# Optimization experiments

Hardware: AMD Instinct MI355X
Metric: run time of the kernel (lower is better)

The kernel has to match this reference:

```python
import jax, jax.numpy as jnp
import numpy as np

B, L, D = 2, 2048, 2048
HQ, HKV = 32, 8
HD = D // HQ            # 64
G = HQ // HKV           # 4


def setup_inputs() -> dict:
    key = jax.random.key(0)
    ks = jax.random.split(key, 9)
    s = 1.0 / np.sqrt(D)
    return {
        "x": jax.random.normal(ks[0], (B, L, D), jnp.float32),
        "Wq": jax.random.normal(ks[1], (D, HQ * HD), jnp.float32) * s,
        "bq": jnp.zeros((HQ * HD,), jnp.float32),
        "Wk": jax.random.normal(ks[2], (D, HKV * HD), jnp.float32) * s,
        "bk": jnp.zeros((HKV * HD,), jnp.float32),
        "Wv": jax.random.normal(ks[3], (D, HKV * HD), jnp.float32) * s,
        "bv": jnp.zeros((HKV * HD,), jnp.float32),
        "Wo": jax.random.normal(ks[4], (HQ * HD, D), jnp.float32) * s,
        "bo": jnp.zeros((D,), jnp.float32),
    }


def reference(x, Wq, bq, Wk, bk, Wv, bv, Wo, bo):
    # projections
    q = x @ Wq + bq                                   # [B, L, HQ*HD]
    k = x @ Wk + bk                                   # [B, L, HKV*HD]
    v = x @ Wv + bv
    # split heads; group q heads by kv head: [B, HKV, G, L, HD]
    q = q.reshape(B, L, HKV, G, HD).transpose(0, 2, 3, 1, 4)
    k = k.reshape(B, L, HKV, HD).transpose(0, 2, 1, 3)   # [B, HKV, L, HD]
    v = v.reshape(B, L, HKV, HD).transpose(0, 2, 1, 3)
    scale = 1.0 / np.sqrt(HD)
    # scores [B, HKV, G, Lq, Lk] -- same math as repeat_kv + matmul
    scores = jnp.einsum('bhgqd,bhkd->bhgqk', q, k) * scale
    attn = jax.nn.softmax(scores, axis=-1)
    ctx = jnp.einsum('bhgqk,bhkd->bhgqd', attn, v)       # [B, HKV, G, L, HD]
    # merge heads back to [B, L, HQ*HD]
    ctx = ctx.transpose(0, 3, 1, 2, 4).reshape(B, L, HQ * HD)
    return ctx @ Wo + bo
```

## Files before the change

### kernel.cpp

```cpp
#include <hip/hip_runtime.h>
#include <cstdint>
#include <cstring>


#define L_SEQ 2048
#define D_MODEL 2048
#define M_ROWS 4096
#define KV_COLS 512
#define ATTN_SCALE 0.18033688011112042f

typedef __bf16 bf16x8 __attribute__((ext_vector_type(8)));
typedef float f32x4 __attribute__((ext_vector_type(4)));
typedef float f32x16 __attribute__((ext_vector_type(16)));

__device__ __forceinline__ f32x4 zero4() {
    f32x4 v; v[0] = 0.f; v[1] = 0.f; v[2] = 0.f; v[3] = 0.f; return v;
}

__device__ __forceinline__ unsigned short f2bf(float x) {
    unsigned u = __builtin_bit_cast(unsigned, x);
    u = (u + 0x7FFFu + ((u >> 16) & 1u)) >> 16;
    return (unsigned short)u;
}

__device__ __forceinline__ unsigned pk_bf16(float a, float b) {
#if __has_builtin(__builtin_amdgcn_cvt_pk_bf16_f32)
    typedef __bf16 bf16x2 __attribute__((ext_vector_type(2)));
    bf16x2 r = __builtin_amdgcn_cvt_pk_bf16_f32(a, b);
    return __builtin_bit_cast(unsigned, r);
#else
    return (unsigned)f2bf(a) | ((unsigned)f2bf(b) << 16);
#endif
}

__device__ __forceinline__ f32x4 mfma16(uint4 a, uint4 b, f32x4 c) {
    return __builtin_amdgcn_mfma_f32_16x16x32_bf16(
        __builtin_bit_cast(bf16x8, a), __builtin_bit_cast(bf16x8, b), c, 0, 0, 0);
}
__device__ __forceinline__ f32x16 mfma32(uint4 a, uint4 b, f32x16 c) {
    return __builtin_amdgcn_mfma_f32_32x32x16_bf16(
        __builtin_bit_cast(bf16x8, a), __builtin_bit_cast(bf16x8, b), c, 0, 0, 0);
}

__device__ __forceinline__ void gl_lds16(const unsigned short* g, unsigned short* l) {
    __builtin_amdgcn_global_load_lds(
        (const __attribute__((address_space(1))) unsigned int*)g,
        (__attribute__((address_space(3))) unsigned int*)l, 16, 0, 0);
}

#if __has_builtin(__builtin_amdgcn_exp2f)
#define EXP2F(x) __builtin_amdgcn_exp2f(x)
#else
#define EXP2F(x) exp2f(x)
#endif


__global__ __launch_bounds__(256) void cast_x_kernel(const float* __restrict__ in,
                                                     unsigned short* __restrict__ out,
                                                     int n4) {
    int i = blockIdx.x * 256 + threadIdx.x;
    if (i >= n4) return;
    float4 v = ((const float4*)in)[i];
    uint2 o;
    o.x = pk_bf16(v.x, v.y);
    o.y = pk_bf16(v.z, v.w);
    ((uint2*)out)[i] = o;
}

__global__ __launch_bounds__(256) void transpose_cast_kernel(const float* __restrict__ in,
                                                             unsigned short* __restrict__ out,
                                                             int N, int row_off) {
    __shared__ float tile[32][33];
    const int n0 = blockIdx.x * 32, k0 = blockIdx.y * 32;
    const int tc = threadIdx.x & 31, tr = threadIdx.x >> 5;
#pragma unroll
    for (int i = 0; i < 4; ++i)
        tile[tr + i * 8][tc] = in[(size_t)(k0 + tr + i * 8) * N + n0 + tc];
    __syncthreads();
#pragma unroll
    for (int i = 0; i < 4; ++i)
        out[(size_t)(row_off + n0 + tr + i * 8) * 2048 + k0 + tc] = f2bf(tile[tc][tr + i * 8]);
}

__global__ __launch_bounds__(256) void transpose_v_kernel(const unsigned short* __restrict__ Vb,
                                                          unsigned short* __restrict__ Vt) {
    __shared__ unsigned short tile[32][33];
    const int c0 = blockIdx.x * 32, l0 = blockIdx.y * 32, b = blockIdx.z;
    const int tc = threadIdx.x & 31, tr = threadIdx.x >> 5;
#pragma unroll
    for (int i = 0; i < 4; ++i)
        tile[tr + i * 8][tc] = Vb[(size_t)(b * 2048 + l0 + tr + i * 8) * KV_COLS + c0 + tc];
    __syncthreads();
#pragma unroll
    for (int i = 0; i < 4; ++i)
        Vt[(size_t)(b * 512 + c0 + tr + i * 8) * 2048 + l0 + tc] = tile[tc][tr + i * 8];
}


__device__ __forceinline__ void gemm_core_2048(const unsigned short* __restrict__ A,
                                               const unsigned short* __restrict__ Bt,
                                               int m_block, int n_block,
                                               unsigned short* smA, unsigned short* smB,
                                               f32x4 acc[4][4]) {
    const int tid = threadIdx.x;
    const int w = tid >> 6, lane = tid & 63;
    const int wm = w >> 1, wn = w & 1;
    const int lr = lane & 15, lg = lane >> 4;

#pragma unroll
    for (int i = 0; i < 4; ++i)
#pragma unroll
        for (int j = 0; j < 4; ++j) acc[i][j] = zero4();

    const int rowA = m_block * 128 + w * 32 + (lane >> 2);
    const int rowB = n_block * 128 + w * 32 + (lane >> 2);
    const int kcol = (lane & 3) * 8;
    const unsigned short* gA0 = A + (size_t)rowA * 2048 + kcol;
    const unsigned short* gA1 = gA0 + (size_t)16 * 2048;
    const unsigned short* gB0 = Bt + (size_t)rowB * 2048 + kcol;
    const unsigned short* gB1 = gB0 + (size_t)16 * 2048;
    unsigned short* lA0 = smA + (w * 32) * 32;
    unsigned short* lA1 = smA + (w * 32 + 16) * 32;
    unsigned short* lB0 = smB + (w * 32) * 32;
    unsigned short* lB1 = smB + (w * 32 + 16) * 32;

    for (int kt = 0; kt < 64; ++kt) {
        gl_lds16(gA0 + kt * 32, lA0);
        gl_lds16(gA1 + kt * 32, lA1);
        gl_lds16(gB0 + kt * 32, lB0);
        gl_lds16(gB1 + kt * 32, lB1);
        __syncthreads();
        uint4 af[4], bfg[4];
#pragma unroll
        for (int i = 0; i < 4; ++i)
            af[i] = *(const uint4*)(smA + (wm * 64 + i * 16 + lr) * 32 + lg * 8);
#pragma unroll
        for (int j = 0; j < 4; ++j)
            bfg[j] = *(const uint4*)(smB + (wn * 64 + j * 16 + lr) * 32 + lg * 8);
#pragma unroll
        for (int i = 0; i < 4; ++i)
#pragma unroll
            for (int j = 0; j < 4; ++j)
                acc[i][j] = mfma16(af[i], bfg[j], acc[i][j]);
        __syncthreads();
    }
}

__global__ __launch_bounds__(256) void gemm_qkv_kernel(
    const unsigned short* __restrict__ Xb, const unsigned short* __restrict__ Wt,
    const float* __restrict__ bq, const float* __restrict__ bk, const float* __restrict__ bv,
    unsigned short* __restrict__ Qb, unsigned short* __restrict__ Kb,
    unsigned short* __restrict__ Vb) {
    __shared__ __align__(16) unsigned short smA[128 * 32];
    __shared__ __align__(16) unsigned short smB[128 * 32];
    f32x4 acc[4][4];
    gemm_core_2048(Xb, Wt, blockIdx.x, blockIdx.y, smA, smB, acc);

    const int tid = threadIdx.x;
    const int w = tid >> 6, lane = tid & 63;
    const int wm = w >> 1, wn = w & 1;
    const int lr = lane & 15, lg = lane >> 4;
    const int nbase = blockIdx.y * 128;

    unsigned short* outp; int ldo, noff; const float* bias; float scale;
    if (nbase < 2048)      { outp = Qb; ldo = 2048; noff = 0;    bias = bq; scale = 1.f; }
    else if (nbase < 2560) { outp = Kb; ldo = 512;  noff = 2048; bias = bk; scale = ATTN_SCALE; }
    else                   { outp = Vb; ldo = 512;  noff = 2560; bias = bv; scale = 1.f; }

#pragma unroll
    for (int i = 0; i < 4; ++i) {
        const int mrow = blockIdx.x * 128 + wm * 64 + i * 16 + lg * 4;
#pragma unroll
        for (int j = 0; j < 4; ++j) {
            const int nloc = nbase + wn * 64 + j * 16 + lr - noff;
            const float bb = bias[nloc];
#pragma unroll
            for (int r = 0; r < 4; ++r)
                outp[(size_t)(mrow + r) * ldo + nloc] = f2bf((acc[i][j][r] + bb) * scale);
        }
    }
}

__global__ __launch_bounds__(256) void gemm_out_kernel(
    const unsigned short* __restrict__ Cb, const unsigned short* __restrict__ Wot,
    const float* __restrict__ bo, float* __restrict__ out) {
    __shared__ __align__(16) unsigned short smA[128 * 32];
    __shared__ __align__(16) unsigned short smB[128 * 32];
    f32x4 acc[4][4];
    gemm_core_2048(Cb, Wot, blockIdx.x, blockIdx.y, smA, smB, acc);

    const int tid = threadIdx.x;
    const int w = tid >> 6, lane = tid & 63;
    const int wm = w >> 1, wn = w & 1;
    const int lr = lane & 15, lg = lane >> 4;

#pragma unroll
    for (int i = 0; i < 4; ++i) {
        const int mrow = blockIdx.x * 128 + wm * 64 + i * 16 + lg * 4;
#pragma unroll
        for (int j = 0; j < 4; ++j) {
            const int ncol = blockIdx.y * 128 + wn * 64 + j * 16 + lr;
            const float bb = bo[ncol];
#pragma unroll
            for (int r = 0; r < 4; ++r)
                out[(size_t)(mrow + r) * 2048 + ncol] = acc[i][j][r] + bb;
        }
    }
}


__global__ __launch_bounds__(256, 2) void attn_kernel(const unsigned short* __restrict__ Qb,
                                                      const unsigned short* __restrict__ Kb,
                                                      const unsigned short* __restrict__ Vtg,
                                                      unsigned short* __restrict__ ctx) {
    __shared__ __align__(16) unsigned short smem[16384];
    unsigned short* ks = smem;
    unsigned short* vt = smem + 8192;

    const int qt = blockIdx.x, hq = blockIdx.y, b = blockIdx.z;
    const int kvh = hq >> 2;
    const int tid = threadIdx.x;
    const int w = tid >> 6, lane = tid & 63;
    const int l31 = lane & 31, h = lane >> 5;

    const int qbase = qt * 256 + w * 64;
    uint4 qf[2][4];
#pragma unroll
    for (int u = 0; u < 2; ++u) {
        const unsigned short* qp =
            Qb + (size_t)(b * L_SEQ + qbase + u * 32 + l31) * 2048 + hq * 64;
#pragma unroll
        for (int dh = 0; dh < 4; ++dh)
            qf[u][dh] = *(const uint4*)(qp + dh * 16 + h * 8);
    }

    f32x16 o00, o01, o10, o11;
#pragma unroll
    for (int r = 0; r < 16; ++r) { o00[r] = 0.f; o01[r] = 0.f; o10[r] = 0.f; o11[r] = 0.f; }
    float l_acc0 = 0.f, l_acc1 = 0.f;

    const size_t kbase = (size_t)(b * L_SEQ) * KV_COLS + kvh * 64;
    const size_t vbase = (size_t)((b * 8 + kvh) * 64) * 2048;

    const int rrk = lane >> 3, cpk = lane & 7;
    const int drv = lane >> 4, cpv = lane & 15;

    for (int t = 0; t < 16; ++t) {
        const int k0 = t * 128;
#pragma unroll
        for (int s = 0; s < 4; ++s) {
            const int blkk = w * 4 + s;
            gl_lds16(Kb + kbase + (size_t)(k0 + blkk * 8 + rrk) * KV_COLS + ((cpk ^ rrk) * 8),
                     ks + blkk * 512);
            const int blkv = w * 4 + s;
            const int d = blkv * 4 + drv;
            gl_lds16(Vtg + vbase + (size_t)d * 2048 + k0 + ((cpv ^ (d & 15)) * 8),
                     vt + blkv * 512);
        }
        __syncthreads();

#pragma unroll
        for (int c = 0; c < 4; ++c) {
            uint4 kf[4];
#pragma unroll
            for (int dh = 0; dh < 4; ++dh)
                kf[dh] = *(const uint4*)&ks[(c * 32 + l31) * 64 +
                                            (((dh * 2 + h) ^ (l31 & 7)) * 8)];
            unsigned E0[4][2], E1[4][2];
#pragma unroll
            for (int u = 0; u < 2; ++u) {
                f32x16 s;
#pragma unroll
                for (int r = 0; r < 16; ++r) s[r] = 0.f;
#pragma unroll
                for (int dh = 0; dh < 4; ++dh) s = mfma32(kf[dh], qf[u][dh], s);
                float lsum = 0.f;
#pragma unroll
                for (int g = 0; g < 4; ++g) {
                    float e0 = EXP2F(s[4 * g + 0]);
                    float e1 = EXP2F(s[4 * g + 1]);
                    float e2 = EXP2F(s[4 * g + 2]);
                    float e3 = EXP2F(s[4 * g + 3]);
                    lsum += (e0 + e1) + (e2 + e3);
                    if (u == 0) { E0[g][0] = pk_bf16(e0, e1); E0[g][1] = pk_bf16(e2, e3); }
                    else        { E1[g][0] = pk_bf16(e0, e1); E1[g][1] = pk_bf16(e2, e3); }
                }
                if (u == 0) l_acc0 += lsum; else l_acc1 += lsum;
            }
            const int posv = (c * 4) ^ (l31 & 15);
#pragma unroll
            for (int tau = 0; tau < 2; ++tau) {
                const int pos = ((c * 4 + tau * 2 + h) ^ (l31 & 15)) * 8;
                uint4 vf0 = *(const uint4*)&vt[(size_t)l31 * 128 + pos];
                uint4 vf1 = *(const uint4*)&vt[(size_t)(32 + l31) * 128 + pos];
                {
                    unsigned pub0 = h ? E0[2 * tau][0] : E0[2 * tau + 1][0];
                    unsigned pub1 = h ? E0[2 * tau][1] : E0[2 * tau + 1][1];
                    unsigned R0 = (unsigned)__shfl_xor((int)pub0, 32, 64);
                    unsigned R1 = (unsigned)__shfl_xor((int)pub1, 32, 64);
                    uint4 pf;
                    pf.x = h ? R0 : E0[2 * tau][0];
                    pf.y = h ? R1 : E0[2 * tau][1];
                    pf.z = h ? E0[2 * tau + 1][0] : R0;
                    pf.w = h ? E0[2 * tau + 1][1] : R1;
                    o00 = mfma32(vf0, pf, o00);
                    o01 = mfma32(vf1, pf, o01);
                }
                {
                    unsigned pub0 = h ? E1[2 * tau][0] : E1[2 * tau + 1][0];
                    unsigned pub1 = h ? E1[2 * tau][1] : E1[2 * tau + 1][1];
                    unsigned R0 = (unsigned)__shfl_xor((int)pub0, 32, 64);
                    unsigned R1 = (unsigned)__shfl_xor((int)pub1, 32, 64);
                    uint4 pf;
                    pf.x = h ? R0 : E1[2 * tau][0];
                    pf.y = h ? R1 : E1[2 * tau][1];
                    pf.z = h ? E1[2 * tau + 1][0] : R0;
                    pf.w = h ? E1[2 * tau + 1][1] : R1;
                    o10 = mfma32(vf0, pf, o10);
                    o11 = mfma32(vf1, pf, o11);
                }
            }
            (void)posv;
        }
        __syncthreads();
    }

    __syncthreads();
    unsigned* ep = (unsigned*)smem + w * 1088;
#pragma unroll
    for (int u = 0; u < 2; ++u) {
        const float la = u ? l_acc1 : l_acc0;
        const float l_tot = la + __shfl_xor(la, 32, 64);
        const float rl = 1.f / l_tot;
#pragma unroll
        for (int dt = 0; dt < 2; ++dt) {
            const f32x16& o = u ? (dt ? o11 : o10) : (dt ? o01 : o00);
#pragma unroll
            for (int g = 0; g < 4; ++g)
#pragma unroll
                for (int p = 0; p < 2; ++p) {
                    const int dv = dt * 16 + 4 * g + 2 * h + p;
                    ep[l31 * 34 + dv] =
                        pk_bf16(o[4 * g + 2 * p] * rl, o[4 * g + 2 * p + 1] * rl);
                }
        }
        __builtin_amdgcn_s_waitcnt(0);
#pragma unroll
        for (int p = 0; p < 4; ++p) {
            const int qr = (lane >> 3) + p * 8;
            const int cch = lane & 7;
            uint4 vv = *(const uint4*)((const unsigned short*)ep + qr * 68 + cch * 8);
            *(uint4*)(ctx + (size_t)(b * L_SEQ + qbase + u * 32 + qr) * 2048 +
                      hq * 64 + cch * 8) = vv;
        }
        __builtin_amdgcn_s_waitcnt(0);
    }
}


extern "C" void kernel_launch(void* const* d_in, const int* in_sizes, int n_in,
                              void* d_out, int out_size, void* d_ws, size_t ws_size,
                              hipStream_t stream) {
    const float* x  = (const float*)d_in[0];
    const float* Wq = (const float*)d_in[1];
    const float* bq = (const float*)d_in[2];
    const float* Wk = (const float*)d_in[3];
    const float* bk = (const float*)d_in[4];
    const float* Wv = (const float*)d_in[5];
    const float* bv = (const float*)d_in[6];
    const float* Wo = (const float*)d_in[7];
    const float* bo = (const float*)d_in[8];
    float* out = (float*)d_out;

    char* ws = (char*)d_ws;
    size_t off = 0;
    auto alloc = [&](size_t bytes) {
        char* p = ws + off;
        off += (bytes + 255) & ~(size_t)255;
        return p;
    };
    unsigned short* Wqkvt = (unsigned short*)alloc((size_t)3072 * 2048 * 2);
    unsigned short* Wot   = (unsigned short*)alloc((size_t)2048 * 2048 * 2);
    unsigned short* Xb    = (unsigned short*)alloc((size_t)M_ROWS * 2048 * 2);
    unsigned short* Qb    = (unsigned short*)alloc((size_t)M_ROWS * 2048 * 2);
    unsigned short* Kb    = (unsigned short*)alloc((size_t)M_ROWS * KV_COLS * 2);
    unsigned short* Vb    = (unsigned short*)alloc((size_t)M_ROWS * KV_COLS * 2);
    unsigned short* Vt    = (unsigned short*)alloc((size_t)M_ROWS * KV_COLS * 2);
    unsigned short* Cb    = Xb;

    cast_x_kernel<<<(M_ROWS * 2048 / 4 + 255) / 256, 256, 0, stream>>>(x, Xb,
                                                                       M_ROWS * 2048 / 4);
    transpose_cast_kernel<<<dim3(64, 64), 256, 0, stream>>>(Wq, Wqkvt, 2048, 0);
    transpose_cast_kernel<<<dim3(16, 64), 256, 0, stream>>>(Wk, Wqkvt, 512, 2048);
    transpose_cast_kernel<<<dim3(16, 64), 256, 0, stream>>>(Wv, Wqkvt, 512, 2560);
    transpose_cast_kernel<<<dim3(64, 64), 256, 0, stream>>>(Wo, Wot, 2048, 0);
    gemm_qkv_kernel<<<dim3(32, 24), 256, 0, stream>>>(Xb, Wqkvt, bq, bk, bv, Qb, Kb, Vb);
    transpose_v_kernel<<<dim3(16, 64, 2), 256, 0, stream>>>(Vb, Vt);
    attn_kernel<<<dim3(8, 32, 2), 256, 0, stream>>>(Qb, Kb, Vt, Cb);
    gemm_out_kernel<<<dim3(32, 16), 256, 0, stream>>>(Cb, Wot, bo, out);
}
```

Before: 348.3 us.

## Double-buffer K/V tiles in attention and split query rows across 8 waves

The attention kernel now runs 512 threads per block, each wave handling 32 query rows instead of 64. This halves the per-wave accumulator registers and raises the occupancy hint. K/V tiles are double-buffered in 64KB of shared memory, so the load for the next tile is issued before computing on the current one. This replaces the old load-sync-compute pattern and removes one barrier per iteration. The cost is doubled LDS per block, which may limit resident blocks, and less register reuse of K/V fragments across query rows.

```diff
diff --git a/kernel.cpp b/kernel.cpp
--- a/kernel.cpp
+++ b/kernel.cpp
@@ -209,13 +209,11 @@
 }
 
 
-__global__ __launch_bounds__(256, 2) void attn_kernel(const unsigned short* __restrict__ Qb,
+__global__ __launch_bounds__(512, 4) void attn_kernel(const unsigned short* __restrict__ Qb,
                                                       const unsigned short* __restrict__ Kb,
                                                       const unsigned short* __restrict__ Vtg,
                                                       unsigned short* __restrict__ ctx) {
-    __shared__ __align__(16) unsigned short smem[16384];
-    unsigned short* ks = smem;
-    unsigned short* vt = smem + 8192;
+    __shared__ __align__(16) unsigned short smem[32768];
 
     const int qt = blockIdx.x, hq = blockIdx.y, b = blockIdx.z;
     const int kvh = hq >> 2;
@@ -223,21 +221,19 @@
     const int w = tid >> 6, lane = tid & 63;
     const int l31 = lane & 31, h = lane >> 5;
 
-    const int qbase = qt * 256 + w * 64;
-    uint4 qf[2][4];
-#pragma unroll
-    for (int u = 0; u < 2; ++u) {
-        const unsigned short* qp =
-            Qb + (size_t)(b * L_SEQ + qbase + u * 32 + l31) * 2048 + hq * 64;
+    const int qbase = qt * 256 + w * 32;
+    uint4 qf[4];
+    {
+        const unsigned short* qp = Qb + (size_t)(b * L_SEQ + qbase + l31) * 2048 + hq * 64;
 #pragma unroll
         for (int dh = 0; dh < 4; ++dh)
-            qf[u][dh] = *(const uint4*)(qp + dh * 16 + h * 8);
-    }
-
-    f32x16 o00, o01, o10, o11;
-#pragma unroll
-    for (int r = 0; r < 16; ++r) { o00[r] = 0.f; o01[r] = 0.f; o10[r] = 0.f; o11[r] = 0.f; }
-    float l_acc0 = 0.f, l_acc1 = 0.f;
+            qf[dh] = *(const uint4*)(qp + dh * 16 + h * 8);
+    }
+
+    f32x16 o0, o1;
+#pragma unroll
+    for (int r = 0; r < 16; ++r) { o0[r] = 0.f; o1[r] = 0.f; }
+    float l_acc = 0.f;
 
     const size_t kbase = (size_t)(b * L_SEQ) * KV_COLS + kvh * 64;
     const size_t vbase = (size_t)((b * 8 + kvh) * 64) * 2048;
@@ -245,115 +241,101 @@
     const int rrk = lane >> 3, cpk = lane & 7;
     const int drv = lane >> 4, cpv = lane & 15;
 
+    unsigned short* ksC = smem;
+    unsigned short* vtC = smem + 8192;
+    unsigned short* ksN = smem + 16384;
+    unsigned short* vtN = smem + 24576;
+
+    auto stage = [&](int T, unsigned short* KS, unsigned short* VT) {
+        const int k0s = T * 128;
+#pragma unroll
+        for (int s = 0; s < 2; ++s) {
+            const int blk = w * 2 + s;
+            gl_lds16(Kb + kbase + (size_t)(k0s + blk * 8 + rrk) * KV_COLS + ((cpk ^ rrk) * 8),
+                     KS + blk * 512);
+            const int d = blk * 4 + drv;
+            gl_lds16(Vtg + vbase + (size_t)d * 2048 + k0s + ((cpv ^ (d & 15)) * 8),
+                     VT + blk * 512);
+        }
+    };
+
+    stage(0, ksC, vtC);
+    __syncthreads();
+
     for (int t = 0; t < 16; ++t) {
-        const int k0 = t * 128;
-#pragma unroll
-        for (int s = 0; s < 4; ++s) {
-            const int blkk = w * 4 + s;
-            gl_lds16(Kb + kbase + (size_t)(k0 + blkk * 8 + rrk) * KV_COLS + ((cpk ^ rrk) * 8),
-                     ks + blkk * 512);
-            const int blkv = w * 4 + s;
-            const int d = blkv * 4 + drv;
-            gl_lds16(Vtg + vbase + (size_t)d * 2048 + k0 + ((cpv ^ (d & 15)) * 8),
-                     vt + blkv * 512);
-        }
-        __syncthreads();
+        if (t < 15) stage(t + 1, ksN, vtN);
 
 #pragma unroll
         for (int c = 0; c < 4; ++c) {
             uint4 kf[4];
 #pragma unroll
             for (int dh = 0; dh < 4; ++dh)
-                kf[dh] = *(const uint4*)&ks[(c * 32 + l31) * 64 +
-                                            (((dh * 2 + h) ^ (l31 & 7)) * 8)];
-            unsigned E0[4][2], E1[4][2];
-#pragma unroll
-            for (int u = 0; u < 2; ++u) {
-                f32x16 s;
-#pragma unroll
-                for (int r = 0; r < 16; ++r) s[r] = 0.f;
-#pragma unroll
-                for (int dh = 0; dh < 4; ++dh) s = mfma32(kf[dh], qf[u][dh], s);
-                float lsum = 0.f;
-#pragma unroll
-                for (int g = 0; g < 4; ++g) {
-                    float e0 = EXP2F(s[4 * g + 0]);
-                    float e1 = EXP2F(s[4 * g + 1]);
-                    float e2 = EXP2F(s[4 * g + 2]);
-                    float e3 = EXP2F(s[4 * g + 3]);
-                    lsum += (e0 + e1) + (e2 + e3);
-                    if (u == 0) { E0[g][0] = pk_bf16(e0, e1); E0[g][1] = pk_bf16(e2, e3); }
-                    else        { E1[g][0] = pk_bf16(e0, e1); E1[g][1] = pk_bf16(e2, e3); }
-                }
-                if (u == 0) l_acc0 += lsum; else l_acc1 += lsum;
+                kf[dh] = *(const uint4*)&ksC[(c * 32 + l31) * 64 +
+                                             (((dh * 2 + h) ^ (l31 & 7)) * 8)];
+            f32x16 s;
+#pragma unroll
+            for (int r = 0; r < 16; ++r) s[r] = 0.f;
+#pragma unroll
+            for (int dh = 0; dh < 4; ++dh) s = mfma32(kf[dh], qf[dh], s);
+            unsigned E[4][2];
+            float lsum = 0.f;
+#pragma unroll
+            for (int g = 0; g < 4; ++g) {
+                float e0 = EXP2F(s[4 * g + 0]);
+                float e1 = EXP2F(s[4 * g + 1]);
+                float e2 = EXP2F(s[4 * g + 2]);
+                float e3 = EXP2F(s[4 * g + 3]);
+                lsum += (e0 + e1) + (e2 + e3);
+                E[g][0] = pk_bf16(e0, e1);
+                E[g][1] = pk_bf16(e2, e3);
             }
-            const int posv = (c * 4) ^ (l31 & 15);
+            l_acc += lsum;
 #pragma unroll
             for (int tau = 0; tau < 2; ++tau) {
                 const int pos = ((c * 4 + tau * 2 + h) ^ (l31 & 15)) * 8;
-                uint4 vf0 = *(const uint4*)&vt[(size_t)l31 * 128 + pos];
-                uint4 vf1 = *(const uint4*)&vt[(size_t)(32 + l31) * 128 + pos];
-                {
-                    unsigned pub0 = h ? E0[2 * tau][0] : E0[2 * tau + 1][0];
-                    unsigned pub1 = h ? E0[2 * tau][1] : E0[2 * tau + 1][1];
-                    unsigned R0 = (unsigned)__shfl_xor((int)pub0, 32, 64);
-                    unsigned R1 = (unsigned)__shfl_xor((int)pub1, 32, 64);
-                    uint4 pf;
-                    pf.x = h ? R0 : E0[2 * tau][0];
-                    pf.y = h ? R1 : E0[2 * tau][1];
-                    pf.z = h ? E0[2 * tau + 1][0] : R0;
-                    pf.w = h ? E0[2 * tau + 1][1] : R1;
-                    o00 = mfma32(vf0, pf, o00);
-                    o01 = mfma32(vf1, pf, o01);
-                }
-                {
-                    unsigned pub0 = h ? E1[2 * tau][0] : E1[2 * tau + 1][0];
-                    unsigned pub1 = h ? E1[2 * tau][1] : E1[2 * tau + 1][1];
-                    unsigned R0 = (unsigned)__shfl_xor((int)pub0, 32, 64);
-                    unsigned R1 = (unsigned)__shfl_xor((int)pub1, 32, 64);
-                    uint4 pf;
-                    pf.x = h ? R0 : E1[2 * tau][0];
-                    pf.y = h ? R1 : E1[2 * tau][1];
-                    pf.z = h ? E1[2 * tau + 1][0] : R0;
-                    pf.w = h ? E1[2 * tau + 1][1] : R1;
-                    o10 = mfma32(vf0, pf, o10);
-                    o11 = mfma32(vf1, pf, o11);
-                }
+                uint4 vf0 = *(const uint4*)&vtC[(size_t)l31 * 128 + pos];
+                uint4 vf1 = *(const uint4*)&vtC[(size_t)(32 + l31) * 128 + pos];
+                unsigned pub0 = h ? E[2 * tau][0] : E[2 * tau + 1][0];
+                unsigned pub1 = h ? E[2 * tau][1] : E[2 * tau + 1][1];
+                unsigned R0 = (unsigned)__shfl_xor((int)pub0, 32, 64);
+                unsigned R1 = (unsigned)__shfl_xor((int)pub1, 32, 64);
+                uint4 pf;
+                pf.x = h ? R0 : E[2 * tau][0];
+                pf.y = h ? R1 : E[2 * tau][1];
+                pf.z = h ? E[2 * tau + 1][0] : R0;
+                pf.w = h ? E[2 * tau + 1][1] : R1;
+                o0 = mfma32(vf0, pf, o0);
+                o1 = mfma32(vf1, pf, o1);
             }
-            (void)posv;
         }
+
         __syncthreads();
-    }
-
-    __syncthreads();
+        unsigned short* tk = ksC; ksC = ksN; ksN = tk;
+        unsigned short* tv = vtC; vtC = vtN; vtN = tv;
+    }
+
     unsigned* ep = (unsigned*)smem + w * 1088;
-#pragma unroll
-    for (int u = 0; u < 2; ++u) {
-        const float la = u ? l_acc1 : l_acc0;
-        const float l_tot = la + __shfl_xor(la, 32, 64);
-        const float rl = 1.f / l_tot;
-#pragma unroll
-        for (int dt = 0; dt < 2; ++dt) {
-            const f32x16& o = u ? (dt ? o11 : o10) : (dt ? o01 : o00);
-#pragma unroll
-            for (int g = 0; g < 4; ++g)
-#pragma unroll
-                for (int p = 0; p < 2; ++p) {
-                    const int dv = dt * 16 + 4 * g + 2 * h + p;
-                    ep[l31 * 34 + dv] =
-                        pk_bf16(o[4 * g + 2 * p] * rl, o[4 * g + 2 * p + 1] * rl);
-                }
-        }
-        __builtin_amdgcn_s_waitcnt(0);
-#pragma unroll
-        for (int p = 0; p < 4; ++p) {
-            const int qr = (lane >> 3) + p * 8;
-            const int cch = lane & 7;
-            uint4 vv = *(const uint4*)((const unsigned short*)ep + qr * 68 + cch * 8);
-            *(uint4*)(ctx + (size_t)(b * L_SEQ + qbase + u * 32 + qr) * 2048 +
-                      hq * 64 + cch * 8) = vv;
-        }
-        __builtin_amdgcn_s_waitcnt(0);
+    const float l_tot = l_acc + __shfl_xor(l_acc, 32, 64);
+    const float rl = 1.f / l_tot;
+#pragma unroll
+    for (int dt = 0; dt < 2; ++dt) {
+        const f32x16& o = dt ? o1 : o0;
+#pragma unroll
+        for (int g = 0; g < 4; ++g)
+#pragma unroll
+            for (int p = 0; p < 2; ++p) {
+                const int dv = dt * 16 + 4 * g + 2 * h + p;
+                ep[l31 * 34 + dv] =
+                    pk_bf16(o[4 * g + 2 * p] * rl, o[4 * g + 2 * p + 1] * rl);
+            }
+    }
+    __builtin_amdgcn_s_waitcnt(0);
+#pragma unroll
+    for (int p = 0; p < 4; ++p) {
+        const int qr = (lane >> 3) + p * 8;
+        const int cch = lane & 7;
+        uint4 vv = *(const uint4*)((const unsigned short*)ep + qr * 68 + cch * 8);
+        *(uint4*)(ctx + (size_t)(b * L_SEQ + qbase + qr) * 2048 + hq * 64 + cch * 8) = vv;
     }
 }
 
@@ -396,6 +378,6 @@
     transpose_cast_kernel<<<dim3(64, 64), 256, 0, stream>>>(Wo, Wot, 2048, 0);
     gemm_qkv_kernel<<<dim3(32, 24), 256, 0, stream>>>(Xb, Wqkvt, bq, bk, bv, Qb, Kb, Vb);
     transpose_v_kernel<<<dim3(16, 64, 2), 256, 0, stream>>>(Vb, Vt);
-    attn_kernel<<<dim3(8, 32, 2), 256, 0, stream>>>(Qb, Kb, Vt, Cb);
+    attn_kernel<<<dim3(8, 32, 2), 512, 0, stream>>>(Qb, Kb, Vt, Cb);
     gemm_out_kernel<<<dim3(32, 16), 256, 0, stream>>>(Cb, Wot, bo, out);
 }
```

Measured after the change: 365.4 us. 4.9% more time.

## Double-buffer K/V tiles in attention and widen blocks to 512 threads

Applied to the files above, without the earlier changes.

Attention kernel now uses 8 waves per block covering 512 queries, with two LDS buffers for K and V tiles. The next tile's load is issued before computing the current one, so global loads overlap with compute and one barrier per iteration is removed. Larger blocks share each K/V tile among more query waves, halving K/V global traffic per query, but LDS grows to 64KB per block, which may limit occupancy, and the grid shrinks to 256 blocks.

```diff
diff --git a/kernel.cpp b/kernel.cpp
--- a/kernel.cpp
+++ b/kernel.cpp
@@ -209,13 +209,11 @@
 }
 
 
-__global__ __launch_bounds__(256, 2) void attn_kernel(const unsigned short* __restrict__ Qb,
+__global__ __launch_bounds__(512, 2) void attn_kernel(const unsigned short* __restrict__ Qb,
                                                       const unsigned short* __restrict__ Kb,
                                                       const unsigned short* __restrict__ Vtg,
                                                       unsigned short* __restrict__ ctx) {
-    __shared__ __align__(16) unsigned short smem[16384];
-    unsigned short* ks = smem;
-    unsigned short* vt = smem + 8192;
+    __shared__ __align__(16) unsigned short smem[32768];
 
     const int qt = blockIdx.x, hq = blockIdx.y, b = blockIdx.z;
     const int kvh = hq >> 2;
@@ -223,7 +221,7 @@
     const int w = tid >> 6, lane = tid & 63;
     const int l31 = lane & 31, h = lane >> 5;
 
-    const int qbase = qt * 256 + w * 64;
+    const int qbase = qt * 512 + w * 64;
     uint4 qf[2][4];
 #pragma unroll
     for (int u = 0; u < 2; ++u) {
@@ -245,27 +243,37 @@
     const int rrk = lane >> 3, cpk = lane & 7;
     const int drv = lane >> 4, cpv = lane & 15;
 
+    unsigned short* ksC = smem;
+    unsigned short* vtC = smem + 8192;
+    unsigned short* ksN = smem + 16384;
+    unsigned short* vtN = smem + 24576;
+
+    auto stage = [&](int T, unsigned short* KS, unsigned short* VT) {
+        const int k0s = T * 128;
+#pragma unroll
+        for (int s = 0; s < 2; ++s) {
+            const int blk = w * 2 + s;
+            gl_lds16(Kb + kbase + (size_t)(k0s + blk * 8 + rrk) * KV_COLS + ((cpk ^ rrk) * 8),
+                     KS + blk * 512);
+            const int d = blk * 4 + drv;
+            gl_lds16(Vtg + vbase + (size_t)d * 2048 + k0s + ((cpv ^ (d & 15)) * 8),
+                     VT + blk * 512);
+        }
+    };
+
+    stage(0, ksC, vtC);
+    __syncthreads();
+
     for (int t = 0; t < 16; ++t) {
-        const int k0 = t * 128;
-#pragma unroll
-        for (int s = 0; s < 4; ++s) {
-            const int blkk = w * 4 + s;
-            gl_lds16(Kb + kbase + (size_t)(k0 + blkk * 8 + rrk) * KV_COLS + ((cpk ^ rrk) * 8),
-                     ks + blkk * 512);
-            const int blkv = w * 4 + s;
-            const int d = blkv * 4 + drv;
-            gl_lds16(Vtg + vbase + (size_t)d * 2048 + k0 + ((cpv ^ (d & 15)) * 8),
-                     vt + blkv * 512);
-        }
-        __syncthreads();
+        if (t < 15) stage(t + 1, ksN, vtN);
 
 #pragma unroll
         for (int c = 0; c < 4; ++c) {
             uint4 kf[4];
 #pragma unroll
             for (int dh = 0; dh < 4; ++dh)
-                kf[dh] = *(const uint4*)&ks[(c * 32 + l31) * 64 +
-                                            (((dh * 2 + h) ^ (l31 & 7)) * 8)];
+                kf[dh] = *(const uint4*)&ksC[(c * 32 + l31) * 64 +
+                                             (((dh * 2 + h) ^ (l31 & 7)) * 8)];
             unsigned E0[4][2], E1[4][2];
 #pragma unroll
             for (int u = 0; u < 2; ++u) {
@@ -287,12 +295,11 @@
                 }
                 if (u == 0) l_acc0 += lsum; else l_acc1 += lsum;
             }
-            const int posv = (c * 4) ^ (l31 & 15);
 #pragma unroll
             for (int tau = 0; tau < 2; ++tau) {
                 const int pos = ((c * 4 + tau * 2 + h) ^ (l31 & 15)) * 8;
-                uint4 vf0 = *(const uint4*)&vt[(size_t)l31 * 128 + pos];
-                uint4 vf1 = *(const uint4*)&vt[(size_t)(32 + l31) * 128 + pos];
+                uint4 vf0 = *(const uint4*)&vtC[(size_t)l31 * 128 + pos];
+                uint4 vf1 = *(const uint4*)&vtC[(size_t)(32 + l31) * 128 + pos];
                 {
                     unsigned pub0 = h ? E0[2 * tau][0] : E0[2 * tau + 1][0];
                     unsigned pub1 = h ? E0[2 * tau][1] : E0[2 * tau + 1][1];
@@ -320,12 +327,13 @@
                     o11 = mfma32(vf1, pf, o11);
                 }
             }
-            (void)posv;
-        }
+        }
+
         __syncthreads();
-    }
-
-    __syncthreads();
+        unsigned short* tk = ksC; ksC = ksN; ksN = tk;
+        unsigned short* tv = vtC; vtC = vtN; vtN = tv;
+    }
+
     unsigned* ep = (unsigned*)smem + w * 1088;
 #pragma unroll
     for (int u = 0; u < 2; ++u) {
@@ -396,6 +404,6 @@
     transpose_cast_kernel<<<dim3(64, 64), 256, 0, stream>>>(Wo, Wot, 2048, 0);
     gemm_qkv_kernel<<<dim3(32, 24), 256, 0, stream>>>(Xb, Wqkvt, bq, bk, bv, Qb, Kb, Vb);
     transpose_v_kernel<<<dim3(16, 64, 2), 256, 0, stream>>>(Vb, Vt);
-    attn_kernel<<<dim3(8, 32, 2), 256, 0, stream>>>(Qb, Kb, Vt, Cb);
+    attn_kernel<<<dim3(4, 32, 2), 512, 0, stream>>>(Qb, Kb, Vt, Cb);
     gemm_out_kernel<<<dim3(32, 16), 256, 0, stream>>>(Cb, Wot, bo, out);
 }
```

Result: no change. 345.5 us (-0.8%).
